# Kernel tuning notes

Measured on AMD Instinct MI355X. Metric: run time of the kernel, lower is better.

## Reference

```python
import jax, jax.numpy as jnp
import numpy as np

N_NODES = 50000
N_EDGES = 800000
N_PAIRS = 200000
IN_DIM = 128
HID = 64
OUT_DIM = 1


def _gat_layer(x, W, a_l, a_r, src, dst, n_nodes):
    # Single-head GAT (DGL-style): z = xW; attention logits from learned
    # left/right vectors; softmax over incoming edges of each dst node.
    z = x @ W                                   # [N, H]
    el = z @ a_l                                # [N]
    er = z @ a_r                                # [N]
    e = jax.nn.leaky_relu(el[src] + er[dst], 0.2)   # [E]
    emax = jax.ops.segment_max(e, dst, num_segments=n_nodes)  # [N]
    ex = jnp.exp(e - emax[dst])                 # [E], stable softmax numerator
    denom = jax.ops.segment_sum(ex, dst, num_segments=n_nodes)  # [N]
    msg = ex[:, None] * z[src]                  # [E, H]
    agg = jax.ops.segment_sum(msg, dst, num_segments=n_nodes)   # [N, H]
    return agg / jnp.maximum(denom, 1e-9)[:, None]


def setup_inputs() -> dict:
    key = jax.random.key(0)
    ks = jax.random.split(key, 10)
    feat = jax.random.normal(ks[0], (N_NODES, IN_DIM), dtype=jnp.float32)
    src = jax.random.randint(ks[1], (N_EDGES,), 0, N_NODES, dtype=jnp.int32)
    dst = jax.random.randint(ks[2], (N_EDGES,), 0, N_NODES, dtype=jnp.int32)
    # query pairs: take existing edges so the has_edges_between mask is true
    pair_src = src[:N_PAIRS]
    pair_dst = dst[:N_PAIRS]
    s1 = 1.0 / np.sqrt(IN_DIM)
    s2 = 1.0 / np.sqrt(HID)
    W1 = jax.random.normal(ks[3], (IN_DIM, HID), dtype=jnp.float32) * s1
    al1 = jax.random.normal(ks[4], (HID,), dtype=jnp.float32) * s2
    ar1 = jax.random.normal(ks[5], (HID,), dtype=jnp.float32) * s2
    W2 = jax.random.normal(ks[6], (HID, HID), dtype=jnp.float32) * s2
    al2 = jax.random.normal(ks[7], (HID,), dtype=jnp.float32) * s2
    ar2 = jax.random.normal(ks[8], (HID,), dtype=jnp.float32) * s2
    Wc = jax.random.normal(ks[9], (2 * HID, OUT_DIM), dtype=jnp.float32) * s2
    bc = jnp.zeros((OUT_DIM,), dtype=jnp.float32)
    return {"feat": feat, "W1": W1, "al1": al1, "ar1": ar1,
            "W2": W2, "al2": al2, "ar2": ar2, "Wc": Wc, "bc": bc,
            "src": src, "dst": dst, "pair_src": pair_src, "pair_dst": pair_dst}


def reference(feat, W1, al1, ar1, W2, al2, ar2, Wc, bc, src, dst, pair_src, pair_dst):
    src = src.astype(jnp.int32)
    dst = dst.astype(jnp.int32)
    # two hetero GAT layers (single ntype -> mean aggregate is identity) + ReLU
    h = jax.nn.relu(_gat_layer(feat, W1, al1, ar1, src, dst, N_NODES))
    h = jax.nn.relu(_gat_layer(h, W2, al2, ar2, src, dst, N_NODES))
    # has_edges_between(pair_src, pair_dst): membership test via sorted edge keys
    ekeys = src.astype(jnp.int64) * N_NODES + dst.astype(jnp.int64)
    skeys = jnp.sort(ekeys)
    pkeys = pair_src.astype(jnp.int64) * N_NODES + pair_dst.astype(jnp.int64)
    idx = jnp.clip(jnp.searchsorted(skeys, pkeys), 0, N_EDGES - 1)
    mask = (skeys[idx] == pkeys)                 # [P] bool
    # gather endpoint embeddings, concat, classify, sigmoid; invalid rows -> 0
    hs = h[pair_src]                             # [P, H]
    hd = h[pair_dst]                             # [P, H]
    h_pair = jnp.concatenate([hs, hd], axis=1)   # [P, 2H]
    out = jax.nn.sigmoid(h_pair @ Wc + bc)       # [P, OUT]
    return out * mask[:, None].astype(out.dtype)
```

## Files before the change

### kernel.cpp

```cpp
#include <hip/hip_runtime.h>
#include <cstdint>

#define N_NODES 50000
#define N_EDGES 800000
#define N_PAIRS 200000
#define IN_DIM 128
#define HID 64
#define N_WAVES_GEMM (N_NODES / 16)
#define NB1 196
#define CHUNK ((N_EDGES + NB1 - 1) / NB1)
#define MHIST (NB1 * NB1)
#define SBG ((MHIST + 255) / 256)
#define MB_GEMM ((N_WAVES_GEMM + 3) / 4)
#define NODE_BLOCKS ((N_NODES + 3) / 4)
#define MEMBER_BLOCKS (N_PAIRS / 32)

typedef __attribute__((ext_vector_type(8))) short bf16x8;
typedef __attribute__((ext_vector_type(4))) float f32x4;

__device__ __forceinline__ unsigned short bf16_rne(float f) {
    unsigned u = __float_as_uint(f);
    unsigned t = u + 0x7FFFu + ((u >> 16) & 1u);
    return (unsigned short)(t >> 16);
}
__device__ __forceinline__ void bf2f(unsigned u, float& a, float& b) {
    a = __uint_as_float(u << 16);
    b = __uint_as_float(u & 0xFFFF0000u);
}

__global__ __launch_bounds__(256) void hist_prep(
    const int* __restrict__ dst, int* __restrict__ histHi,
    const float* __restrict__ W1, const float* __restrict__ W2,
    unsigned short* __restrict__ w1hi, unsigned short* __restrict__ w1lo,
    unsigned short* __restrict__ w2hi, unsigned short* __restrict__ w2lo)
{
    const int t = threadIdx.x, b = blockIdx.x;
    if (b < NB1) {
        __shared__ int hist[256];
        hist[t] = 0; __syncthreads();
        const int beg = b * CHUNK, end = min(beg + CHUNK, N_EDGES);
        for (int e = beg + t; e < end; e += 256) atomicAdd(&hist[dst[e] >> 8], 1);
        __syncthreads();
        if (t < NB1) histHi[t * NB1 + b] = hist[t];
    } else {
        int tid = (b - NB1) * 256 + t;
        if (tid < 8192) {
            int jj = tid & 7, lane = (tid >> 3) & 63, tt = (tid >> 9) & 3, ks = tid >> 11;
            int k = ks * 32 + (lane >> 4) * 8 + jj;
            int n = tt * 16 + (lane & 15);
            float f = W1[k * HID + n];
            unsigned short hi = bf16_rne(f);
            float fhi = __uint_as_float(((unsigned)hi) << 16);
            w1hi[tid] = hi;
            w1lo[tid] = bf16_rne(f - fhi);
        }
        if (tid < 4096) {
            int jj = tid & 7, lane = (tid >> 3) & 63, tt = (tid >> 9) & 3, ks = tid >> 11;
            int k = ks * 32 + (lane >> 4) * 8 + jj;
            int n = tt * 16 + (lane & 15);
            float f = W2[k * HID + n];
            unsigned short hi = bf16_rne(f);
            float fhi = __uint_as_float(((unsigned)hi) << 16);
            w2hi[tid] = hi;
            w2lo[tid] = bf16_rne(f - fhi);
        }
    }
}

__device__ __forceinline__ void gemm1_body(
    int wave, int lane,
    const float* __restrict__ x,
    const unsigned short* __restrict__ whi, const unsigned short* __restrict__ wlo,
    const float* __restrict__ al, const float* __restrict__ ar,
    unsigned short* __restrict__ z, float* __restrict__ el, float* __restrict__ er)
{
    const int i0 = wave * 16;
    const int m = lane & 15, quad = lane >> 4;
    f32x4 acc[4] = {{0.f,0.f,0.f,0.f},{0.f,0.f,0.f,0.f},{0.f,0.f,0.f,0.f},{0.f,0.f,0.f,0.f}};
    const float* xrow = x + (size_t)(i0 + m) * IN_DIM;

    #pragma unroll 1
    for (int ks = 0; ks < 4; ++ks) {
        const float4 xv0 = *(const float4*)&xrow[ks * 32 + quad * 8];
        const float4 xv1 = *(const float4*)&xrow[ks * 32 + quad * 8 + 4];
        float xs[8] = {xv0.x, xv0.y, xv0.z, xv0.w, xv1.x, xv1.y, xv1.z, xv1.w};
        bf16x8 ahi, alo;
        #pragma unroll
        for (int jj = 0; jj < 8; ++jj) {
            unsigned short hb = bf16_rne(xs[jj]);
            float fhi = __uint_as_float(((unsigned)hb) << 16);
            ahi[jj] = (short)hb;
            alo[jj] = (short)bf16_rne(xs[jj] - fhi);
        }
        #pragma unroll
        for (int t = 0; t < 4; ++t) {
            const bf16x8 bhi = *(const bf16x8*)&whi[(((ks * 4 + t) * 64) + lane) * 8];
            const bf16x8 blo = *(const bf16x8*)&wlo[(((ks * 4 + t) * 64) + lane) * 8];
            acc[t] = __builtin_amdgcn_mfma_f32_16x16x32_bf16(ahi, bhi, acc[t], 0, 0, 0);
            acc[t] = __builtin_amdgcn_mfma_f32_16x16x32_bf16(ahi, blo, acc[t], 0, 0, 0);
            acc[t] = __builtin_amdgcn_mfma_f32_16x16x32_bf16(alo, bhi, acc[t], 0, 0, 0);
        }
    }
    #pragma unroll
    for (int r = 0; r < 4; ++r) {
        const int row = quad * 4 + r;
        float se = 0.f, sr = 0.f;
        #pragma unroll
        for (int t = 0; t < 4; ++t) {
            float v = acc[t][r];
            z[(size_t)(i0 + row) * HID + t * 16 + m] = bf16_rne(v);
            se = fmaf(v, al[t * 16 + m], se);
            sr = fmaf(v, ar[t * 16 + m], sr);
        }
        #pragma unroll
        for (int off = 1; off < 16; off <<= 1) {
            se += __shfl_xor(se, off, 64);
            sr += __shfl_xor(sr, off, 64);
        }
        if (m == 0) { el[i0 + row] = se; er[i0 + row] = sr; }
    }
}

__global__ __launch_bounds__(256) void scan_gemm1(
    int* __restrict__ histHi, int* __restrict__ bsums,
    const float* __restrict__ x,
    const unsigned short* __restrict__ whi, const unsigned short* __restrict__ wlo,
    const float* __restrict__ al, const float* __restrict__ ar,
    unsigned short* __restrict__ z, float* __restrict__ el, float* __restrict__ er)
{
    const int b = blockIdx.x;
    if (b < SBG) {
        __shared__ int sh[256];
        const int t = threadIdx.y * 64 + threadIdx.x;
        const int i = b * 256 + t;
        int v = (i < MHIST) ? histHi[i] : 0;
        sh[t] = v; __syncthreads();
        #pragma unroll
        for (int off = 1; off < 256; off <<= 1) {
            int x2 = sh[t];
            int a = (t >= off) ? sh[t - off] : 0;
            __syncthreads();
            sh[t] = x2 + a;
            __syncthreads();
        }
        if (i < MHIST) histHi[i] = sh[t] - v;
        if (t == 255) bsums[b] = sh[255];
    } else {
        const int wave = (b - SBG) * 4 + threadIdx.y;
        if (wave < N_WAVES_GEMM)
            gemm1_body(wave, threadIdx.x, x, whi, wlo, al, ar, z, el, er);
    }
}

__device__ __forceinline__ void scan_bsums(const int* __restrict__ bsums,
                                           int* sh, int* exb, int t)
{
    int v = (t < SBG) ? bsums[t] : 0;
    sh[t] = v; __syncthreads();
    #pragma unroll
    for (int off = 1; off < 256; off <<= 1) {
        int x = sh[t];
        int a = (t >= off) ? sh[t - off] : 0;
        __syncthreads();
        sh[t] = x + a;
        __syncthreads();
    }
    exb[t] = sh[t] - v;
    __syncthreads();
}

__global__ __launch_bounds__(256) void scatter_hi(
    const int* __restrict__ src, const int* __restrict__ dst,
    const int* __restrict__ histEx, const int* __restrict__ bsums,
    unsigned* __restrict__ pairs)
{
    __shared__ int sh[256], exb[256], base[256];
    const int t = threadIdx.x, b = blockIdx.x;
    scan_bsums(bsums, sh, exb, t);
    if (t < NB1) {
        int idx = t * NB1 + b;
        base[t] = histEx[idx] + exb[idx >> 8];
    }
    __syncthreads();
    const int beg = b * CHUNK, end = min(beg + CHUNK, N_EDGES);
    for (int e = beg + t; e < end; e += 256) {
        int s = src[e], d = dst[e];
        int pos = atomicAdd(&base[d >> 8], 1);
        pairs[pos] = ((unsigned)s << 16) | (unsigned)d;
    }
}

__global__ __launch_bounds__(256) void seg_sort(
    const unsigned* __restrict__ pairs, const int* __restrict__ histEx,
    const int* __restrict__ bsums,
    int* __restrict__ row_start, int* __restrict__ csr_src)
{
    __shared__ int sh[256], exb[256], hist[256], sc[256], offs[256];
    const int t = threadIdx.x, b = blockIdx.x;
    scan_bsums(bsums, sh, exb, t);
    const int i0 = b * NB1;
    const int segStart = histEx[i0] + exb[i0 >> 8];
    int segEnd = N_EDGES;
    if (b < NB1 - 1) {
        const int i1 = (b + 1) * NB1;
        segEnd = histEx[i1] + exb[i1 >> 8];
    }
    hist[t] = 0; __syncthreads();
    for (int i = segStart + t; i < segEnd; i += 256)
        atomicAdd(&hist[pairs[i] & 255], 1);
    __syncthreads();
    int v = hist[t]; sc[t] = v; __syncthreads();
    #pragma unroll
    for (int off = 1; off < 256; off <<= 1) {
        int x = sc[t];
        int a = (t >= off) ? sc[t - off] : 0;
        __syncthreads();
        sc[t] = x + a;
        __syncthreads();
    }
    const int excl = sc[t] - v;
    offs[t] = segStart + excl;
    const int node = b * 256 + t;
    if (node <= N_NODES) row_start[node] = segStart + excl;
    __syncthreads();
    for (int i = segStart + t; i < segEnd; i += 256) {
        unsigned p = pairs[i];
        int pos = atomicAdd(&offs[p & 255], 1);
        csr_src[pos] = (int)(p >> 16);
    }
}

template <bool LAST>
__device__ __forceinline__ void agg_body(
    int i, int lane,
    const int* __restrict__ row_start, const int* __restrict__ csr_src,
    const float* __restrict__ el, const float* __restrict__ er,
    const unsigned short* __restrict__ z, unsigned short* __restrict__ h,
    const float* __restrict__ Wc, float* __restrict__ as, float* __restrict__ ad)
{
    const int rb = row_start[i], re = row_start[i + 1];
    const float er_i = er[i];
    const int es = lane >> 3;
    const int fl = lane & 7;

    float acc[8] = {0.f,0.f,0.f,0.f,0.f,0.f,0.f,0.f};
    float den = 0.f;

    int eA = rb + es;        bool vA = eA < re;
    int eB = eA + 8;         bool vB = eB < re;
    int sA = vA ? csr_src[eA] : 0;
    int sB = vB ? csr_src[eB] : 0;
    float elA = el[sA];
    uint4 zA = ((const uint4*)(z + (size_t)sA * HID))[fl];

    for (int e0 = rb; e0 < re; e0 += 8) {
        const int eC = e0 + 16 + es;
        const bool vC = eC < re;
        const int sC = vC ? csr_src[eC] : 0;
        const float elB = el[sB];
        const uint4 zB = ((const uint4*)(z + (size_t)sB * HID))[fl];

        float x = elA + er_i;
        float lr = x > 0.f ? x : 0.2f * x;
        float ex = vA ? __expf(lr) : 0.f;
        float z0, z1, z2, z3, z4, z5, z6, z7;
        bf2f(zA.x, z0, z1); bf2f(zA.y, z2, z3);
        bf2f(zA.z, z4, z5); bf2f(zA.w, z6, z7);
        acc[0] = fmaf(ex, z0, acc[0]); acc[1] = fmaf(ex, z1, acc[1]);
        acc[2] = fmaf(ex, z2, acc[2]); acc[3] = fmaf(ex, z3, acc[3]);
        acc[4] = fmaf(ex, z4, acc[4]); acc[5] = fmaf(ex, z5, acc[5]);
        acc[6] = fmaf(ex, z6, acc[6]); acc[7] = fmaf(ex, z7, acc[7]);
        den += ex;

        sA = sB; vA = vB; elA = elB; zA = zB;
        sB = sC; vB = vC;
    }
    #pragma unroll
    for (int off = 8; off < 64; off <<= 1) {
        #pragma unroll
        for (int q = 0; q < 8; ++q) acc[q] += __shfl_xor(acc[q], off, 64);
        den += __shfl_xor(den, off, 64);
    }
    if (es == 0) {
        float inv = 1.f / fmaxf(den, 1e-9f);
        float hv[8];
        #pragma unroll
        for (int q = 0; q < 8; ++q) hv[q] = fmaxf(acc[q] * inv, 0.f);
        if (LAST) {
            float ps = 0.f, pd = 0.f;
            #pragma unroll
            for (int q = 0; q < 8; ++q) {
                ps = fmaf(hv[q], Wc[fl * 8 + q], ps);
                pd = fmaf(hv[q], Wc[HID + fl * 8 + q], pd);
            }
            #pragma unroll
            for (int off = 1; off < 8; off <<= 1) {
                ps += __shfl_xor(ps, off, 64);
                pd += __shfl_xor(pd, off, 64);
            }
            if (fl == 0) { as[i] = ps; ad[i] = pd; }
        } else {
            unsigned short o[8];
            #pragma unroll
            for (int q = 0; q < 8; ++q) o[q] = bf16_rne(hv[q]);
            uint4 pk;
            pk.x = (unsigned)o[0] | ((unsigned)o[1] << 16);
            pk.y = (unsigned)o[2] | ((unsigned)o[3] << 16);
            pk.z = (unsigned)o[4] | ((unsigned)o[5] << 16);
            pk.w = (unsigned)o[6] | ((unsigned)o[7] << 16);
            ((uint4*)(h + (size_t)i * HID))[fl] = pk;
        }
    }
}

__global__ __launch_bounds__(256) void agg1_member(
    const int* __restrict__ row_start, const int* __restrict__ csr_src,
    const float* __restrict__ el, const float* __restrict__ er,
    const unsigned short* __restrict__ z, unsigned short* __restrict__ h,
    const int* __restrict__ ps, const int* __restrict__ pd,
    int* __restrict__ found)
{
    const int lane = threadIdx.x, b = blockIdx.x;
    if (b < NODE_BLOCKS) {
        const int i = b * 4 + threadIdx.y;
        if (i < N_NODES)
            agg_body<false>(i, lane, row_start, csr_src, el, er, z, h,
                            nullptr, nullptr, nullptr);
    } else {
        const int r = lane & 7, g = lane >> 3;
        const int p = (b - NODE_BLOCKS) * 32 + threadIdx.y * 8 + g;
        const int s = ps[p], d = pd[p];
        const int rb = row_start[d], re = row_start[d + 1];
        int f = 0;
        for (int e = rb + r; e < re; e += 8) f |= (csr_src[e] == s) ? 1 : 0;
        #pragma unroll
        for (int off = 1; off < 8; off <<= 1) f |= __shfl_xor(f, off, 64);
        if (r == 0) found[p] = f;
    }
}

__global__ __launch_bounds__(256) void gemm_mfma_b(
    const unsigned short* __restrict__ x,
    const unsigned short* __restrict__ whi, const unsigned short* __restrict__ wlo,
    const float* __restrict__ al, const float* __restrict__ ar,
    unsigned short* __restrict__ z, float* __restrict__ el, float* __restrict__ er)
{
    const int lane = threadIdx.x;
    const int wave = blockIdx.x * 4 + threadIdx.y;
    if (wave >= N_WAVES_GEMM) return;
    const int i0 = wave * 16;
    const int m = lane & 15, quad = lane >> 4;

    f32x4 acc[4] = {{0.f,0.f,0.f,0.f},{0.f,0.f,0.f,0.f},{0.f,0.f,0.f,0.f},{0.f,0.f,0.f,0.f}};
    const unsigned short* xrow = x + (size_t)(i0 + m) * HID;

    #pragma unroll 1
    for (int ks = 0; ks < 2; ++ks) {
        const bf16x8 a = *(const bf16x8*)&xrow[ks * 32 + quad * 8];
        #pragma unroll
        for (int t = 0; t < 4; ++t) {
            const bf16x8 bhi = *(const bf16x8*)&whi[(((ks * 4 + t) * 64) + lane) * 8];
            const bf16x8 blo = *(const bf16x8*)&wlo[(((ks * 4 + t) * 64) + lane) * 8];
            acc[t] = __builtin_amdgcn_mfma_f32_16x16x32_bf16(a, bhi, acc[t], 0, 0, 0);
            acc[t] = __builtin_amdgcn_mfma_f32_16x16x32_bf16(a, blo, acc[t], 0, 0, 0);
        }
    }
    #pragma unroll
    for (int r = 0; r < 4; ++r) {
        const int row = quad * 4 + r;
        float se = 0.f, sr = 0.f;
        #pragma unroll
        for (int t = 0; t < 4; ++t) {
            float v = acc[t][r];
            z[(size_t)(i0 + row) * HID + t * 16 + m] = bf16_rne(v);
            se = fmaf(v, al[t * 16 + m], se);
            sr = fmaf(v, ar[t * 16 + m], sr);
        }
        #pragma unroll
        for (int off = 1; off < 16; off <<= 1) {
            se += __shfl_xor(se, off, 64);
            sr += __shfl_xor(sr, off, 64);
        }
        if (m == 0) { el[i0 + row] = se; er[i0 + row] = sr; }
    }
}

__global__ __launch_bounds__(256) void agg2(
    const int* __restrict__ row_start, const int* __restrict__ csr_src,
    const float* __restrict__ el, const float* __restrict__ er,
    const unsigned short* __restrict__ z, const float* __restrict__ Wc,
    float* __restrict__ as, float* __restrict__ ad)
{
    const int i = blockIdx.x * 4 + threadIdx.y;
    if (i < N_NODES)
        agg_body<true>(i, threadIdx.x, row_start, csr_src, el, er, z,
                       nullptr, Wc, as, ad);
}

__global__ __launch_bounds__(256) void pair_tiny(
    const int* __restrict__ ps, const int* __restrict__ pd,
    const float* __restrict__ as, const float* __restrict__ ad,
    const float* __restrict__ bc, const int* __restrict__ found,
    float* __restrict__ out)
{
    const int p = blockIdx.x * 256 + threadIdx.x;
    if (p >= N_PAIRS) return;
    float v = as[ps[p]] + ad[pd[p]] + bc[0];
    float sg = 1.f / (1.f + __expf(-v));
    out[p] = found[p] ? sg : 0.f;
}

extern "C" void kernel_launch(void* const* d_in, const int* in_sizes, int n_in,
                              void* d_out, int out_size, void* d_ws, size_t ws_size,
                              hipStream_t stream)
{
    const float* feat = (const float*)d_in[0];
    const float* W1   = (const float*)d_in[1];
    const float* al1  = (const float*)d_in[2];
    const float* ar1  = (const float*)d_in[3];
    const float* W2   = (const float*)d_in[4];
    const float* al2  = (const float*)d_in[5];
    const float* ar2  = (const float*)d_in[6];
    const float* Wc   = (const float*)d_in[7];
    const float* bc   = (const float*)d_in[8];
    const int* src    = (const int*)d_in[9];
    const int* dst    = (const int*)d_in[10];
    const int* psrc   = (const int*)d_in[11];
    const int* pdst   = (const int*)d_in[12];
    float* out = (float*)d_out;

    char* ws = (char*)d_ws;
    unsigned short* z  = (unsigned short*)ws;  ws += (size_t)N_NODES * HID * 2;
    unsigned short* h1 = (unsigned short*)ws;  ws += (size_t)N_NODES * HID * 2;
    float* el = (float*)ws;               ws += (size_t)N_NODES * 4;
    float* er = (float*)ws;               ws += (size_t)N_NODES * 4;
    float* as = (float*)ws;               ws += (size_t)N_NODES * 4;
    float* ad = (float*)ws;               ws += (size_t)N_NODES * 4;
    int* row_start = (int*)ws;            ws += (size_t)(N_NODES + 1) * 4;
    int* histHi = (int*)ws;               ws += (size_t)MHIST * 4;
    int* bsumsA = (int*)ws;               ws += (size_t)(SBG + 1) * 4;
    int* found = (int*)ws;                ws += (size_t)N_PAIRS * 4;
    ws = (char*)(((uintptr_t)ws + 255) & ~(uintptr_t)255);
    unsigned* pairs = (unsigned*)ws;      ws += (size_t)N_EDGES * 4;
    int* csr_src = (int*)ws;              ws += (size_t)N_EDGES * 4;
    unsigned short* w1hi = (unsigned short*)ws;  ws += 8192 * 2;
    unsigned short* w1lo = (unsigned short*)ws;  ws += 8192 * 2;
    unsigned short* w2hi = (unsigned short*)ws;  ws += 4096 * 2;
    unsigned short* w2lo = (unsigned short*)ws;  ws += 4096 * 2;

    dim3 b64x4(64, 4);

    hist_prep<<<NB1 + 32, 256, 0, stream>>>(dst, histHi, W1, W2, w1hi, w1lo, w2hi, w2lo);
    scan_gemm1<<<SBG + MB_GEMM, b64x4, 0, stream>>>(histHi, bsumsA,
        feat, w1hi, w1lo, al1, ar1, z, el, er);
    scatter_hi<<<NB1, 256, 0, stream>>>(src, dst, histHi, bsumsA, pairs);
    seg_sort<<<NB1, 256, 0, stream>>>(pairs, histHi, bsumsA, row_start, csr_src);
    agg1_member<<<NODE_BLOCKS + MEMBER_BLOCKS, b64x4, 0, stream>>>(
        row_start, csr_src, el, er, z, h1, psrc, pdst, found);
    gemm_mfma_b<<<MB_GEMM, b64x4, 0, stream>>>(h1, w2hi, w2lo, al2, ar2, z, el, er);
    agg2<<<NODE_BLOCKS, b64x4, 0, stream>>>(row_start, csr_src, el, er, z, Wc, as, ad);
    pair_tiny<<<(N_PAIRS + 255) / 256, 256, 0, stream>>>(psrc, pdst, as, ad, bc, found, out);
}
```

Before: 194.0 us.

## Regroup kernel co-scheduling and store CSR source indices as 16-bit

```diff
diff --git a/kernel.cpp b/kernel.cpp
--- a/kernel.cpp
+++ b/kernel.cpp
@@ -67,6 +67,43 @@
     }
 }
 
+__global__ __launch_bounds__(256) void scan1g(
+    int* __restrict__ histHi, int* __restrict__ bsums)
+{
+    __shared__ int sh[256];
+    const int t = threadIdx.x;
+    const int i = blockIdx.x * 256 + t;
+    int v = (i < MHIST) ? histHi[i] : 0;
+    sh[t] = v; __syncthreads();
+    #pragma unroll
+    for (int off = 1; off < 256; off <<= 1) {
+        int x = sh[t];
+        int a = (t >= off) ? sh[t - off] : 0;
+        __syncthreads();
+        sh[t] = x + a;
+        __syncthreads();
+    }
+    if (i < MHIST) histHi[i] = sh[t] - v;
+    if (t == 255) bsums[blockIdx.x] = sh[255];
+}
+
+__device__ __forceinline__ void scan_bsums(const int* __restrict__ bsums,
+                                           int* sh, int* exb, int t)
+{
+    int v = (t < SBG) ? bsums[t] : 0;
+    sh[t] = v; __syncthreads();
+    #pragma unroll
+    for (int off = 1; off < 256; off <<= 1) {
+        int x = sh[t];
+        int a = (t >= off) ? sh[t - off] : 0;
+        __syncthreads();
+        sh[t] = x + a;
+        __syncthreads();
+    }
+    exb[t] = sh[t] - v;
+    __syncthreads();
+}
+
 __device__ __forceinline__ void gemm1_body(
     int wave, int lane,
     const float* __restrict__ x,
@@ -121,79 +158,42 @@
     }
 }
 
-__global__ __launch_bounds__(256) void scan_gemm1(
-    int* __restrict__ histHi, int* __restrict__ bsums,
+__global__ __launch_bounds__(256) void scatter_gemm1(
+    const int* __restrict__ src, const int* __restrict__ dst,
+    const int* __restrict__ histEx, const int* __restrict__ bsums,
+    unsigned* __restrict__ pairs,
     const float* __restrict__ x,
     const unsigned short* __restrict__ whi, const unsigned short* __restrict__ wlo,
     const float* __restrict__ al, const float* __restrict__ ar,
     unsigned short* __restrict__ z, float* __restrict__ el, float* __restrict__ er)
 {
     const int b = blockIdx.x;
-    if (b < SBG) {
-        __shared__ int sh[256];
+    if (b < NB1) {
+        __shared__ int sh[256], exb[256], base[256];
         const int t = threadIdx.y * 64 + threadIdx.x;
-        const int i = b * 256 + t;
-        int v = (i < MHIST) ? histHi[i] : 0;
-        sh[t] = v; __syncthreads();
-        #pragma unroll
-        for (int off = 1; off < 256; off <<= 1) {
-            int x2 = sh[t];
-            int a = (t >= off) ? sh[t - off] : 0;
-            __syncthreads();
-            sh[t] = x2 + a;
-            __syncthreads();
-        }
-        if (i < MHIST) histHi[i] = sh[t] - v;
-        if (t == 255) bsums[b] = sh[255];
+        scan_bsums(bsums, sh, exb, t);
+        if (t < NB1) {
+            int idx = t * NB1 + b;
+            base[t] = histEx[idx] + exb[idx >> 8];
+        }
+        __syncthreads();
+        const int beg = b * CHUNK, end = min(beg + CHUNK, N_EDGES);
+        for (int e = beg + t; e < end; e += 256) {
+            int s = src[e], d = dst[e];
+            int pos = atomicAdd(&base[d >> 8], 1);
+            pairs[pos] = ((unsigned)s << 16) | (unsigned)d;
+        }
     } else {
-        const int wave = (b - SBG) * 4 + threadIdx.y;
+        const int wave = (b - NB1) * 4 + threadIdx.y;
         if (wave < N_WAVES_GEMM)
             gemm1_body(wave, threadIdx.x, x, whi, wlo, al, ar, z, el, er);
-    }
-}
-
-__device__ __forceinline__ void scan_bsums(const int* __restrict__ bsums,
-                                           int* sh, int* exb, int t)
-{
-    int v = (t < SBG) ? bsums[t] : 0;
-    sh[t] = v; __syncthreads();
-    #pragma unroll
-    for (int off = 1; off < 256; off <<= 1) {
-        int x = sh[t];
-        int a = (t >= off) ? sh[t - off] : 0;
-        __syncthreads();
-        sh[t] = x + a;
-        __syncthreads();
-    }
-    exb[t] = sh[t] - v;
-    __syncthreads();
-}
-
-__global__ __launch_bounds__(256) void scatter_hi(
-    const int* __restrict__ src, const int* __restrict__ dst,
-    const int* __restrict__ histEx, const int* __restrict__ bsums,
-    unsigned* __restrict__ pairs)
-{
-    __shared__ int sh[256], exb[256], base[256];
-    const int t = threadIdx.x, b = blockIdx.x;
-    scan_bsums(bsums, sh, exb, t);
-    if (t < NB1) {
-        int idx = t * NB1 + b;
-        base[t] = histEx[idx] + exb[idx >> 8];
-    }
-    __syncthreads();
-    const int beg = b * CHUNK, end = min(beg + CHUNK, N_EDGES);
-    for (int e = beg + t; e < end; e += 256) {
-        int s = src[e], d = dst[e];
-        int pos = atomicAdd(&base[d >> 8], 1);
-        pairs[pos] = ((unsigned)s << 16) | (unsigned)d;
     }
 }
 
 __global__ __launch_bounds__(256) void seg_sort(
     const unsigned* __restrict__ pairs, const int* __restrict__ histEx,
     const int* __restrict__ bsums,
-    int* __restrict__ row_start, int* __restrict__ csr_src)
+    int* __restrict__ row_start, unsigned short* __restrict__ csr_src)
 {
     __shared__ int sh[256], exb[256], hist[256], sc[256], offs[256];
     const int t = threadIdx.x, b = blockIdx.x;
@@ -226,14 +226,14 @@
     for (int i = segStart + t; i < segEnd; i += 256) {
         unsigned p = pairs[i];
         int pos = atomicAdd(&offs[p & 255], 1);
-        csr_src[pos] = (int)(p >> 16);
+        csr_src[pos] = (unsigned short)(p >> 16);
     }
 }
 
 template <bool LAST>
 __device__ __forceinline__ void agg_body(
     int i, int lane,
-    const int* __restrict__ row_start, const int* __restrict__ csr_src,
+    const int* __restrict__ row_start, const unsigned short* __restrict__ csr_src,
     const float* __restrict__ el, const float* __restrict__ er,
     const unsigned short* __restrict__ z, unsigned short* __restrict__ h,
     const float* __restrict__ Wc, float* __restrict__ as, float* __restrict__ ad)
@@ -248,15 +248,15 @@
 
     int eA = rb + es;        bool vA = eA < re;
     int eB = eA + 8;         bool vB = eB < re;
-    int sA = vA ? csr_src[eA] : 0;
-    int sB = vB ? csr_src[eB] : 0;
+    int sA = vA ? (int)csr_src[eA] : 0;
+    int sB = vB ? (int)csr_src[eB] : 0;
     float elA = el[sA];
     uint4 zA = ((const uint4*)(z + (size_t)sA * HID))[fl];
 
     for (int e0 = rb; e0 < re; e0 += 8) {
         const int eC = e0 + 16 + es;
         const bool vC = eC < re;
-        const int sC = vC ? csr_src[eC] : 0;
+        const int sC = vC ? (int)csr_src[eC] : 0;
         const float elB = el[sB];
         const uint4 zB = ((const uint4*)(z + (size_t)sB * HID))[fl];
 
@@ -313,80 +313,77 @@
     }
 }
 
-__global__ __launch_bounds__(256) void agg1_member(
-    const int* __restrict__ row_start, const int* __restrict__ csr_src,
+__global__ __launch_bounds__(256) void agg1(
+    const int* __restrict__ row_start, const unsigned short* __restrict__ csr_src,
     const float* __restrict__ el, const float* __restrict__ er,
-    const unsigned short* __restrict__ z, unsigned short* __restrict__ h,
-    const int* __restrict__ ps, const int* __restrict__ pd,
-    int* __restrict__ found)
+    const unsigned short* __restrict__ z, unsigned short* __restrict__ h)
+{
+    const int i = blockIdx.x * 4 + threadIdx.y;
+    if (i < N_NODES)
+        agg_body<false>(i, threadIdx.x, row_start, csr_src, el, er, z, h,
+                        nullptr, nullptr, nullptr);
+}
+
+__global__ __launch_bounds__(256) void gemm2_member(
+    const unsigned short* __restrict__ x,
+    const unsigned short* __restrict__ whi, const unsigned short* __restrict__ wlo,
+    const float* __restrict__ al, const float* __restrict__ ar,
+    unsigned short* __restrict__ z, float* __restrict__ el, float* __restrict__ er,
+    const int* __restrict__ row_start, const unsigned short* __restrict__ csr_src,
+    const int* __restrict__ ps, const int* __restrict__ pd, int* __restrict__ found)
 {
     const int lane = threadIdx.x, b = blockIdx.x;
-    if (b < NODE_BLOCKS) {
-        const int i = b * 4 + threadIdx.y;
-        if (i < N_NODES)
-            agg_body<false>(i, lane, row_start, csr_src, el, er, z, h,
-                            nullptr, nullptr, nullptr);
+    if (b < MB_GEMM) {
+        const int wave = b * 4 + threadIdx.y;
+        if (wave >= N_WAVES_GEMM) return;
+        const int i0 = wave * 16;
+        const int m = lane & 15, quad = lane >> 4;
+        f32x4 acc[4] = {{0.f,0.f,0.f,0.f},{0.f,0.f,0.f,0.f},{0.f,0.f,0.f,0.f},{0.f,0.f,0.f,0.f}};
+        const unsigned short* xrow = x + (size_t)(i0 + m) * HID;
+        #pragma unroll 1
+        for (int ks = 0; ks < 2; ++ks) {
+            const bf16x8 a = *(const bf16x8*)&xrow[ks * 32 + quad * 8];
+            #pragma unroll
+            for (int t = 0; t < 4; ++t) {
+                const bf16x8 bhi = *(const bf16x8*)&whi[(((ks * 4 + t) * 64) + lane) * 8];
+                const bf16x8 blo = *(const bf16x8*)&wlo[(((ks * 4 + t) * 64) + lane) * 8];
+                acc[t] = __builtin_amdgcn_mfma_f32_16x16x32_bf16(a, bhi, acc[t], 0, 0, 0);
+                acc[t] = __builtin_amdgcn_mfma_f32_16x16x32_bf16(a, blo, acc[t], 0, 0, 0);
+            }
+        }
+        #pragma unroll
+        for (int r = 0; r < 4; ++r) {
+            const int row = quad * 4 + r;
+            float se = 0.f, sr = 0.f;
+            #pragma unroll
+            for (int t = 0; t < 4; ++t) {
+                float v = acc[t][r];
+                z[(size_t)(i0 + row) * HID + t * 16 + m] = bf16_rne(v);
+                se = fmaf(v, al[t * 16 + m], se);
+                sr = fmaf(v, ar[t * 16 + m], sr);
+            }
+            #pragma unroll
+            for (int off = 1; off < 16; off <<= 1) {
+                se += __shfl_xor(se, off, 64);
+                sr += __shfl_xor(sr, off, 64);
+            }
+            if (m == 0) { el[i0 + row] = se; er[i0 + row] = sr; }
+        }
     } else {
         const int r = lane & 7, g = lane >> 3;
-        const int p = (b - NODE_BLOCKS) * 32 + threadIdx.y * 8 + g;
+        const int p = (b - MB_GEMM) * 32 + threadIdx.y * 8 + g;
         const int s = ps[p], d = pd[p];
         const int rb = row_start[d], re = row_start[d + 1];
         int f = 0;
-        for (int e = rb + r; e < re; e += 8) f |= (csr_src[e] == s) ? 1 : 0;
+        for (int e = rb + r; e < re; e += 8) f |= ((int)csr_src[e] == s) ? 1 : 0;
         #pragma unroll
         for (int off = 1; off < 8; off <<= 1) f |= __shfl_xor(f, off, 64);
         if (r == 0) found[p] = f;
     }
 }
 
-__global__ __launch_bounds__(256) void gemm_mfma_b(
-    const unsigned short* __restrict__ x,
-    const unsigned short* __restrict__ whi, const unsigned short* __restrict__ wlo,
-    const float* __restrict__ al, const float* __restrict__ ar,
-    unsigned short* __restrict__ z, float* __restrict__ el, float* __restrict__ er)
-{
-    const int lane = threadIdx.x;
-    const int wave = blockIdx.x * 4 + threadIdx.y;
-    if (wave >= N_WAVES_GEMM) return;
-    const int i0 = wave * 16;
-    const int m = lane & 15, quad = lane >> 4;
-
-    f32x4 acc[4] = {{0.f,0.f,0.f,0.f},{0.f,0.f,0.f,0.f},{0.f,0.f,0.f,0.f},{0.f,0.f,0.f,0.f}};
-    const unsigned short* xrow = x + (size_t)(i0 + m) * HID;
-
-    #pragma unroll 1
-    for (int ks = 0; ks < 2; ++ks) {
-        const bf16x8 a = *(const bf16x8*)&xrow[ks * 32 + quad * 8];
-        #pragma unroll
-        for (int t = 0; t < 4; ++t) {
-            const bf16x8 bhi = *(const bf16x8*)&whi[(((ks * 4 + t) * 64) + lane) * 8];
-            const bf16x8 blo = *(const bf16x8*)&wlo[(((ks * 4 + t) * 64) + lane) * 8];
-            acc[t] = __builtin_amdgcn_mfma_f32_16x16x32_bf16(a, bhi, acc[t], 0, 0, 0);
-            acc[t] = __builtin_amdgcn_mfma_f32_16x16x32_bf16(a, blo, acc[t], 0, 0, 0);
-        }
-    }
-    #pragma unroll
-    for (int r = 0; r < 4; ++r) {
-        const int row = quad * 4 + r;
-        float se = 0.f, sr = 0.f;
-        #pragma unroll
-        for (int t = 0; t < 4; ++t) {
-            float v = acc[t][r];
-            z[(size_t)(i0 + row) * HID + t * 16 + m] = bf16_rne(v);
-            se = fmaf(v, al[t * 16 + m], se);
-            sr = fmaf(v, ar[t * 16 + m], sr);
-        }
-        #pragma unroll
-        for (int off = 1; off < 16; off <<= 1) {
-            se += __shfl_xor(se, off, 64);
-            sr += __shfl_xor(sr, off, 64);
-        }
-        if (m == 0) { el[i0 + row] = se; er[i0 + row] = sr; }
-    }
-}
-
 __global__ __launch_bounds__(256) void agg2(
-    const int* __restrict__ row_start, const int* __restrict__ csr_src,
+    const int* __restrict__ row_start, const unsigned short* __restrict__ csr_src,
     const float* __restrict__ el, const float* __restrict__ er,
     const unsigned short* __restrict__ z, const float* __restrict__ Wc,
     float* __restrict__ as, float* __restrict__ ad)
@@ -442,7 +439,8 @@
     int* found = (int*)ws;                ws += (size_t)N_PAIRS * 4;
     ws = (char*)(((uintptr_t)ws + 255) & ~(uintptr_t)255);
     unsigned* pairs = (unsigned*)ws;      ws += (size_t)N_EDGES * 4;
-    int* csr_src = (int*)ws;              ws += (size_t)N_EDGES * 4;
+    unsigned short* csr_src = (unsigned short*)ws;  ws += (size_t)N_EDGES * 2;
+    ws = (char*)(((uintptr_t)ws + 255) & ~(uintptr_t)255);
     unsigned short* w1hi = (unsigned short*)ws;  ws += 8192 * 2;
     unsigned short* w1lo = (unsigned short*)ws;  ws += 8192 * 2;
     unsigned short* w2hi = (unsigned short*)ws;  ws += 4096 * 2;
@@ -451,13 +449,13 @@
     dim3 b64x4(64, 4);
 
     hist_prep<<<NB1 + 32, 256, 0, stream>>>(dst, histHi, W1, W2, w1hi, w1lo, w2hi, w2lo);
-    scan_gemm1<<<SBG + MB_GEMM, b64x4, 0, stream>>>(histHi, bsumsA,
+    scan1g<<<SBG, 256, 0, stream>>>(histHi, bsumsA);
+    scatter_gemm1<<<NB1 + MB_GEMM, b64x4, 0, stream>>>(src, dst, histHi, bsumsA, pairs,
         feat, w1hi, w1lo, al1, ar1, z, el, er);
-    scatter_hi<<<NB1, 256, 0, stream>>>(src, dst, histHi, bsumsA, pairs);
     seg_sort<<<NB1, 256, 0, stream>>>(pairs, histHi, bsumsA, row_start, csr_src);
-    agg1_member<<<NODE_BLOCKS + MEMBER_BLOCKS, b64x4, 0, stream>>>(
-        row_start, csr_src, el, er, z, h1, psrc, pdst, found);
-    gemm_mfma_b<<<MB_GEMM, b64x4, 0, stream>>>(h1, w2hi, w2lo, al2, ar2, z, el, er);
+    agg1<<<NODE_BLOCKS, b64x4, 0, stream>>>(row_start, csr_src, el, er, z, h1);
+    gemm2_member<<<MB_GEMM + MEMBER_BLOCKS, b64x4, 0, stream>>>(h1, w2hi, w2lo,
+        al2, ar2, z, el, er, row_start, csr_src, psrc, pdst, found);
     agg2<<<NODE_BLOCKS, b64x4, 0, stream>>>(row_start, csr_src, el, er, z, Wc, as, ad);
     pair_tiny<<<(N_PAIRS + 255) / 256, 256, 0, stream>>>(psrc, pdst, as, ad, bc, found, out);
 }
```

Result: no change. 193.8 us (median of 2 runs) (-0.1%).
